# Kernel optimization log

Measured on AMD Instinct MI355X. Metric: run time of the kernel, lower is better.

Reference implementation:

```python
import jax, jax.numpy as jnp
import numpy as np

B, T, N, C = 64, 256, 21, 3
HID, HEADS, HDIM, DOUT = 128, 4, 32, 256
CDIM, DMODEL = 64, 256
DINNER, DSTATE, DCONV, DTRANK, L = 512, 16, 4, 16, 4
NSIGNS, NHS, NLOC, NMOV, NORI = 2000, 40, 20, 20, 8
TEMP = 0.07

def _ln(x, w):
    mu = x.mean(-1, keepdims=True)
    var = ((x - mu) ** 2).mean(-1, keepdims=True)
    return (x - mu) / jnp.sqrt(var + 1e-5) * w

def _silu(x):
    return x * jax.nn.sigmoid(x)

def _causal_conv(u, w, b):  # u:(B,T,D), depthwise causal conv, w:(D,K)
    K = w.shape[1]
    up = jnp.pad(u, ((0, 0), (K - 1, 0), (0, 0)))
    y = sum(up[:, k:k + u.shape[1], :] * w[:, k] for k in range(K))
    return y + b

def _scan(u, dt, Bm, Cm, A, Dp):  # selective SSM scan; u,dt:(B,T,Di), Bm,Cm:(B,T,Ds)
    def step(h, xs):
        dt_t, b_t, c_t, u_t = xs
        dA = jnp.exp(dt_t[..., None] * A)                       # (B,Di,Ds)
        dBu = dt_t[..., None] * b_t[:, None, :] * u_t[..., None]
        h = dA * h + dBu
        y = jnp.einsum('bds,bs->bd', h, c_t)
        return h, y
    h0 = jnp.zeros((u.shape[0], A.shape[0], A.shape[1]), u.dtype)
    xs = (dt.swapaxes(0, 1), Bm.swapaxes(0, 1), Cm.swapaxes(0, 1), u.swapaxes(0, 1))
    _, ys = jax.lax.scan(step, h0, xs)
    return ys.swapaxes(0, 1) + u * Dp

def _cos_logits(f, p):
    fn = f / (jnp.linalg.norm(f, axis=-1, keepdims=True) + 1e-8)
    pn = p / (jnp.linalg.norm(p, axis=-1, keepdims=True) + 1e-8)
    return fn @ pn.T / TEMP

def _forward(x, agan_w_in, agan_b_in, agan_w_gat, agan_a_src, agan_a_dst,
             agan_w_out, agan_b_out, pdm_w, pdm_b, pdm_w_fuse, pdm_b_fuse,
             ssm_ln_w, ssm_in_proj, ssm_conv_w, ssm_conv_b, ssm_x_proj,
             ssm_dt_w, ssm_dt_b, ssm_A_log, ssm_D, ssm_out_proj,
             hpc_w_sign, hpc_b_sign, sign_protos, proto_hs, proto_loc,
             proto_mov, proto_ori):
    # ---- AGAN: multi-head graph attention over N landmarks per frame ----
    h0 = jax.nn.relu(x @ agan_w_in + agan_b_in)                  # (B,T,N,HID)
    h = jnp.einsum('btni,hio->btnho', h0, agan_w_gat)            # (B,T,N,H,O)
    src = jnp.einsum('btnho,ho->btnh', h, agan_a_src)
    dst = jnp.einsum('btnho,ho->btnh', h, agan_a_dst)
    e = jax.nn.leaky_relu(src[:, :, :, None, :] + dst[:, :, None, :, :], 0.2)  # (B,T,Ni,Nj,H)
    alpha = jax.nn.softmax(e, axis=3)
    agg = jnp.einsum('btijh,btjho->btiho', alpha, h).reshape(h0.shape)
    feat = jax.nn.relu(h0 + agg)
    spatial = (feat @ agan_w_out + agan_b_out).mean(axis=2)      # (B,T,DOUT)
    # ---- PDM: 4 phonological component projections + fusion ----
    comps = jax.nn.relu(jnp.einsum('btd,kdc->btkc', spatial, pdm_w) + pdm_b)  # (B,T,4,CDIM)
    fused = comps.reshape(B, T, 4 * CDIM) @ pdm_w_fuse + pdm_b_fuse           # (B,T,DMODEL)
    # ---- BiSSM: bidirectional selective SSM layers with residuals ----
    xx = fused
    for l in range(L):
        xn = _ln(xx, ssm_ln_w[l])
        ysum = 0.0
        for d in range(2):
            u_in = xn if d == 0 else xn[:, ::-1]
            xz = u_in @ ssm_in_proj[l, d]
            u, z = xz[..., :DINNER], xz[..., DINNER:]
            u = _silu(_causal_conv(u, ssm_conv_w[l, d], ssm_conv_b[l, d]))
            xdbl = u @ ssm_x_proj[l, d]
            dt = jax.nn.softplus(xdbl[..., :DTRANK] @ ssm_dt_w[l, d] + ssm_dt_b[l, d])
            Bm = xdbl[..., DTRANK:DTRANK + DSTATE]
            Cm = xdbl[..., DTRANK + DSTATE:]
            A = -jnp.exp(ssm_A_log[l, d])
            y = _scan(u, dt, Bm, Cm, A, ssm_D[l, d]) * _silu(z)
            y = y @ ssm_out_proj[l, d]
            ysum = ysum + (y if d == 0 else y[:, ::-1])
        xx = xx + ysum
    temporal = xx
    # ---- HPC: prototype classifier ----
    emb = temporal.mean(axis=1) @ hpc_w_sign + hpc_b_sign        # (B,DMODEL)
    logits = _cos_logits(emb, sign_protos)                       # (B,NSIGNS)
    pooled_c = comps.mean(axis=1)                                # (B,4,CDIM)
    sims = tuple(_cos_logits(pooled_c[:, k], p)
                 for k, p in enumerate((proto_hs, proto_loc, proto_mov, proto_ori)))
    return (logits, emb) + sims

def setup_inputs():
    key = jax.random.key(0)
    ks = iter(jax.random.split(key, 40))
    def rn(shape, scale):
        return jax.random.normal(next(ks), shape, jnp.float32) * scale
    inp = {}
    inp['x'] = rn((B, T, N, C), 1.0)
    inp['agan_w_in'] = rn((C, HID), C ** -0.5)
    inp['agan_b_in'] = jnp.zeros((HID,), jnp.float32)
    inp['agan_w_gat'] = rn((HEADS, HID, HDIM), HID ** -0.5)
    inp['agan_a_src'] = rn((HEADS, HDIM), 0.1)
    inp['agan_a_dst'] = rn((HEADS, HDIM), 0.1)
    inp['agan_w_out'] = rn((HID, DOUT), HID ** -0.5)
    inp['agan_b_out'] = jnp.zeros((DOUT,), jnp.float32)
    inp['pdm_w'] = rn((4, DOUT, CDIM), DOUT ** -0.5)
    inp['pdm_b'] = jnp.zeros((4, CDIM), jnp.float32)
    inp['pdm_w_fuse'] = rn((4 * CDIM, DMODEL), (4 * CDIM) ** -0.5)
    inp['pdm_b_fuse'] = jnp.zeros((DMODEL,), jnp.float32)
    inp['ssm_ln_w'] = jnp.ones((L, DMODEL), jnp.float32)
    inp['ssm_in_proj'] = rn((L, 2, DMODEL, 2 * DINNER), DMODEL ** -0.5)
    inp['ssm_conv_w'] = rn((L, 2, DINNER, DCONV), DCONV ** -0.5)
    inp['ssm_conv_b'] = jnp.zeros((L, 2, DINNER), jnp.float32)
    inp['ssm_x_proj'] = rn((L, 2, DINNER, DTRANK + 2 * DSTATE), DINNER ** -0.5)
    inp['ssm_dt_w'] = rn((L, 2, DTRANK, DINNER), DTRANK ** -0.5)
    inp['ssm_dt_b'] = jnp.full((L, 2, DINNER), -4.6, jnp.float32)  # softplus ~ 0.01
    a = jnp.log(jnp.tile(jnp.arange(1, DSTATE + 1, dtype=jnp.float32)[None, :], (DINNER, 1)))
    inp['ssm_A_log'] = jnp.tile(a[None, None], (L, 2, 1, 1))
    inp['ssm_D'] = jnp.ones((L, 2, DINNER), jnp.float32)
    inp['ssm_out_proj'] = rn((L, 2, DINNER, DMODEL), DINNER ** -0.5)
    inp['hpc_w_sign'] = rn((DMODEL, DMODEL), DMODEL ** -0.5)
    inp['hpc_b_sign'] = jnp.zeros((DMODEL,), jnp.float32)
    inp['sign_protos'] = rn((NSIGNS, DMODEL), 1.0)
    inp['proto_hs'] = rn((NHS, CDIM), 1.0)
    inp['proto_loc'] = rn((NLOC, CDIM), 1.0)
    inp['proto_mov'] = rn((NMOV, CDIM), 1.0)
    inp['proto_ori'] = rn((NORI, CDIM), 1.0)
    return inp

def reference(x, agan_w_in, agan_b_in, agan_w_gat, agan_a_src, agan_a_dst,
              agan_w_out, agan_b_out, pdm_w, pdm_b, pdm_w_fuse, pdm_b_fuse,
              ssm_ln_w, ssm_in_proj, ssm_conv_w, ssm_conv_b, ssm_x_proj,
              ssm_dt_w, ssm_dt_b, ssm_A_log, ssm_D, ssm_out_proj,
              hpc_w_sign, hpc_b_sign, sign_protos, proto_hs, proto_loc,
              proto_mov, proto_ori):
    return _forward(x, agan_w_in, agan_b_in, agan_w_gat, agan_a_src, agan_a_dst,
                    agan_w_out, agan_b_out, pdm_w, pdm_b, pdm_w_fuse, pdm_b_fuse,
                    ssm_ln_w, ssm_in_proj, ssm_conv_w, ssm_conv_b, ssm_x_proj,
                    ssm_dt_w, ssm_dt_b, ssm_A_log, ssm_D, ssm_out_proj,
                    hpc_w_sign, hpc_b_sign, sign_protos, proto_hs, proto_loc,
                    proto_mov, proto_ori)
```

## Files before the change

### kernel.cpp

```cpp
#include <hip/hip_runtime.h>
#include <hip/hip_bf16.h>
#include <math.h>

#define BB 64
#define TT 256
#define NNODE 21
#define HID 128
#define DMODEL 256
#define DINNER 512
#define NSIGNS 2000
#define BTT (BB*TT)

typedef unsigned short u16;
typedef unsigned int u32;
typedef __attribute__((ext_vector_type(8))) short short8;
typedef __attribute__((ext_vector_type(4))) float f32x4;

template<int V> struct IC { static constexpr int v = V; };

__device__ __forceinline__ float siluf(float x){ return x/(1.f+expf(-x)); }
__device__ __forceinline__ u16 f2bf(float x){ __hip_bfloat16 h = __float2bfloat16(x); return *(u16*)&h; }
__device__ __forceinline__ u32 pk2bf(float a, float b){
  float2 f2; f2.x = a; f2.y = b;
  __hip_bfloat162 h2 = __float22bfloat162_rn(f2);
  return *(u32*)&h2;
}
__device__ __forceinline__ float bf2f(u16 u){ return __uint_as_float(((u32)u)<<16); }
__device__ __forceinline__ void gload16(const u16* g, u16* l){
  __builtin_amdgcn_global_load_lds((const __attribute__((address_space(1))) void*)g,
                                   (__attribute__((address_space(3))) void*)l, 16, 0, 0);
}

__global__ __launch_bounds__(256) void transpose_w_kernel(
    const float* __restrict__ in_proj, const float* __restrict__ out_proj,
    const float* __restrict__ x_proj, const float* __restrict__ w_out,
    const float* __restrict__ pdm_w, const float* __restrict__ w_fuse,
    const float* __restrict__ w_gat, u16* __restrict__ dst)
{
  __shared__ short tl[64*66];
  int bx = blockIdx.x, tid = threadIdx.x;
  const float* S = nullptr; size_t soff = 0; int lds = 0, Nsrc = 0;
  size_t doff = 0; int ldd = 0, Nout = 0;
  int tn = 0, tk = 0;
  bool zero = false;
  if (bx < 512) {
    int j = bx >> 5, tt = bx & 31;
    int l = j >> 2, d = j & 1, zh = (j >> 1) & 1;
    tn = tt >> 2; tk = tt & 3;
    S = in_proj; soff = ((size_t)(l*2+d)*256)*1024 + zh*512; lds = 1024; Nsrc = 512;
    doff = (size_t)l*524288 + (size_t)(zh*1024 + d*512)*256; ldd = 256; Nout = 512;
  } else if (bx < 768) {
    int j = (bx-512) >> 5, tt = (bx-512) & 31;
    int l = j >> 1, d = j & 1;
    tn = tt >> 3; tk = tt & 7;
    S = out_proj; soff = (size_t)(l*2+d)*512*256; lds = 256; Nsrc = 256;
    doff = 2097152 + (size_t)l*262144 + d*512; ldd = 1024; Nout = 256;
  } else if (bx < 896) {
    int j = (bx-768) >> 3, tt = (bx-768) & 7;
    int l = j >> 2, sub = j & 3;
    tn = 0; tk = tt;
    if (sub < 2) {
      int d = sub;
      S = x_proj; soff = (size_t)(l*2+d)*512*48; lds = 48; Nsrc = 48;
      doff = 3145728 + (size_t)l*131072 + (size_t)(d*64)*1024 + d*512; ldd = 1024; Nout = 64;
    } else {
      int d = sub-2; zero = true;
      doff = 3145728 + (size_t)l*131072 + (size_t)(d*64)*1024 + (1-d)*512; ldd = 1024; Nout = 64;
    }
  } else if (bx < 904) {
    int tt = bx-896; tn = tt>>1; tk = tt&1;
    S = w_out; soff = 0; lds = 256; Nsrc = 256;
    doff = 3670016; ldd = 128; Nout = 256;
  } else if (bx < 920) {
    int j = (bx-904)>>2, tt = (bx-904)&3;
    tn = 0; tk = tt;
    S = pdm_w; soff = (size_t)j*16384; lds = 64; Nsrc = 64;
    doff = 3702784 + (size_t)j*16384; ldd = 256; Nout = 64;
  } else if (bx < 936) {
    int tt = bx-920; tn = tt>>2; tk = tt&3;
    S = w_fuse; soff = 0; lds = 256; Nsrc = 256;
    doff = 3768320; ldd = 256; Nout = 256;
  } else {
    int j = (bx-936)>>1, tt = (bx-936)&1;
    tn = 0; tk = tt;
    S = w_gat; soff = (size_t)j*4096; lds = 32; Nsrc = 32;
    doff = 3833856 + (size_t)j*4096; ldd = 128; Nout = 32;
  }
  int n0 = tn*64, k0 = tk*64;
  if (!zero) {
    #pragma unroll
    for (int i=0;i<16;++i){
      int kk = i*4 + (tid>>6), nn = tid&63;
      float v = (n0+nn < Nsrc) ? S[soff + (size_t)(k0+kk)*lds + n0+nn] : 0.f;
      tl[nn*66+kk] = (short)f2bf(v);
    }
    __syncthreads();
    #pragma unroll
    for (int i=0;i<16;++i){
      int nn = i*4 + (tid>>6), kk = tid&63;
      if (n0+nn < Nout) dst[doff + (size_t)(n0+nn)*ldd + k0+kk] = (u16)tl[nn*66+kk];
    }
  } else {
    #pragma unroll
    for (int i=0;i<16;++i){
      int nn = i*4 + (tid>>6), kk = tid&63;
      if (n0+nn < Nout) dst[doff + (size_t)(n0+nn)*ldd + k0+kk] = 0;
    }
  }
}

__global__ __launch_bounds__(256) void agan_kernel(
    const float* __restrict__ x, const float* __restrict__ w_in, const float* __restrict__ b_in,
    const u16* __restrict__ bpt, const float* __restrict__ a_src, const float* __restrict__ a_dst,
    u16* __restrict__ fsum_out)
{
  int bt = blockIdx.x;
  int tid = threadIdx.x;
  int lane = tid & 63, wid = tid >> 6;
  int lr = lane & 15, lq = lane >> 4;
  __shared__ float xv[NNODE][4];
  __shared__ __align__(16) short sh0[32*136];
  __shared__ __align__(16) short hmT[128*40];
  __shared__ __align__(16) short alb[4*32*40];
  __shared__ float sd[2][NNODE][4];
  __shared__ float sm[4][NNODE];
  short8 bp[4][2];
  #pragma unroll
  for (int ks=0;ks<4;++ks)
    #pragma unroll
    for (int ct=0;ct<2;++ct)
      bp[ks][ct] = *(const short8*)(bpt + (size_t)(wid*32+ct*16+lr)*128 + ks*32 + lq*8);
  float as0 = a_src[wid*32 + lr],      as1 = a_src[wid*32 + 16 + lr];
  float ad0 = a_dst[wid*32 + lr],      ad1 = a_dst[wid*32 + 16 + lr];
  if (tid < NNODE*3) xv[tid/3][tid%3] = x[(size_t)bt*63 + tid];
  __syncthreads();
  for (int idx = tid; idx < 32*128; idx += 256) {
    int n = idx >> 7, i = idx & 127;
    float v = 0.f;
    if (n < NNODE)
      v = fmaxf(b_in[i] + xv[n][0]*w_in[i] + xv[n][1]*w_in[128+i] + xv[n][2]*w_in[256+i], 0.f);
    sh0[n*136 + i] = (short)f2bf(v);
  }
  __syncthreads();
  {
    f32x4 g00={},g01={},g10={},g11={};
    #pragma unroll
    for (int ks=0;ks<4;++ks){
      short8 a0 = *(const short8*)&sh0[(lr   )*136 + ks*32 + lq*8];
      short8 a1 = *(const short8*)&sh0[(16+lr)*136 + ks*32 + lq*8];
      g00 = __builtin_amdgcn_mfma_f32_16x16x32_bf16(a0, bp[ks][0], g00, 0,0,0);
      g01 = __builtin_amdgcn_mfma_f32_16x16x32_bf16(a0, bp[ks][1], g01, 0,0,0);
      g10 = __builtin_amdgcn_mfma_f32_16x16x32_bf16(a1, bp[ks][0], g10, 0,0,0);
      g11 = __builtin_amdgcn_mfma_f32_16x16x32_bf16(a1, bp[ks][1], g11, 0,0,0);
    }
    f32x4 gg[2][2] = {{g00,g01},{g10,g11}};
    #pragma unroll
    for (int mt=0;mt<2;++mt)
      #pragma unroll
      for (int ct=0;ct<2;++ct){
        int col = wid*32 + ct*16 + lr;
        int row0 = mt*16 + lq*4;
        u32 w0 = pk2bf(gg[mt][ct][0], gg[mt][ct][1]);
        u32 w1 = pk2bf(gg[mt][ct][2], gg[mt][ct][3]);
        *(uint2*)&hmT[col*40 + row0] = make_uint2(w0,w1);
      }
    #pragma unroll
    for (int mt=0;mt<2;++mt)
      #pragma unroll
      for (int r=0;r<4;++r){
        float ps = gg[mt][0][r]*as0 + gg[mt][1][r]*as1;
        float pd = gg[mt][0][r]*ad0 + gg[mt][1][r]*ad1;
        #pragma unroll
        for (int off=1; off<16; off<<=1){
          ps += __shfl_xor(ps, off);
          pd += __shfl_xor(pd, off);
        }
        int n = mt*16 + lq*4 + r;
        if (lr == 0 && n < NNODE){ sd[0][n][wid] = ps; sd[1][n][wid] = pd; }
      }
  }
  __syncthreads();
  if (tid < 84) {
    int i = tid >> 2, h = tid & 3;
    float sv = sd[0][i][h], m = -1e30f;
    #pragma unroll
    for (int j=0;j<NNODE;++j){
      float e = sv + sd[1][j][h];
      e = e>=0.f ? e : 0.2f*e;
      m = fmaxf(m,e);
    }
    sm[h][i] = m;
  }
  __syncthreads();
  for (int idx = tid; idx < 84*32; idx += 256) {
    int j = idx & 31, ih = idx >> 5;
    int i = ih >> 2, h = ih & 3;
    float ex = 0.f;
    if (j < NNODE){
      float e = sd[0][i][h] + sd[1][j][h];
      e = e>=0.f ? e : 0.2f*e;
      ex = __expf(e - sm[h][i]);
    }
    alb[(h*32+i)*40 + j] = (short)f2bf(ex);
  }
  __syncthreads();
  if (tid < 84) {
    int i = tid >> 2, h = tid & 3;
    const short* row = &alb[(h*32+i)*40];
    float s = 0.f;
    #pragma unroll
    for (int j=0;j<NNODE;++j) s += bf2f((u16)row[j]);
    sm[h][i] = 1.f/s;
  }
  __syncthreads();
  {
    int h = wid;
    short8 a0 = *(const short8*)&alb[(h*32 + lr     )*40 + lq*8];
    short8 a1 = *(const short8*)&alb[(h*32 + 16 + lr)*40 + lq*8];
    short8 b0 = *(const short8*)&hmT[(h*32 + lr     )*40 + lq*8];
    short8 b1 = *(const short8*)&hmT[(h*32 + 16 + lr)*40 + lq*8];
    f32x4 c00={},c01={},c10={},c11={};
    c00 = __builtin_amdgcn_mfma_f32_16x16x32_bf16(a0,b0,c00,0,0,0);
    c01 = __builtin_amdgcn_mfma_f32_16x16x32_bf16(a0,b1,c01,0,0,0);
    c10 = __builtin_amdgcn_mfma_f32_16x16x32_bf16(a1,b0,c10,0,0,0);
    c11 = __builtin_amdgcn_mfma_f32_16x16x32_bf16(a1,b1,c11,0,0,0);
    f32x4 cc[2][2] = {{c00,c01},{c10,c11}};
    #pragma unroll
    for (int ct=0; ct<2; ++ct){
      int col = h*32 + ct*16 + lr;
      float s = 0.f;
      #pragma unroll
      for (int mt=0; mt<2; ++mt)
        #pragma unroll
        for (int r=0;r<4;++r){
          int n = mt*16 + lq*4 + r;
          if (n < NNODE)
            s += fmaxf(bf2f((u16)sh0[n*136+col]) + cc[mt][ct][r]*sm[h][n], 0.f);
        }
      s += __shfl_xor(s, 16);
      s += __shfl_xor(s, 32);
      if (lq == 0) fsum_out[(size_t)bt*128 + col] = f2bf(s*(1.f/21.f));
    }
  }
}

template<int ACC, int BIAS, int RELU, int SM>
__global__ __launch_bounds__(256) void gemm_bf16_kernel(
    const u16* __restrict__ A, const u16* __restrict__ BT, const float* __restrict__ bias,
    float* __restrict__ C, u16* __restrict__ C2,
    int M, int N, int K, int lda)
{
  __shared__ __align__(16) short Asl[8192];
  __shared__ __align__(16) short Bsl[8192];
  int tid = threadIdx.x;
  int lane = tid & 63, wid = tid >> 6;
  int wm = wid >> 1, wn = wid & 1;
  int row0 = blockIdx.y*128, col0 = blockIdx.x*128;
  const u16* Ab = A  + (size_t)row0*lda;
  const u16* Bb = BT + (size_t)col0*K;
  f32x4 acc[4][4] = {};
  int lrow = lane & 15, lk = (lane>>4)*8;
  for (int k0 = 0; k0 < K; k0 += 64) {
    #pragma unroll
    for (int is=0; is<4; ++is){
      int li = is*256 + tid;
      int row = li >> 3;
      int c8  = (li & 7) ^ (row & 7);
      gload16(Ab + (size_t)row*lda + k0 + c8*8, (u16*)Asl + ((is<<8)+(wid<<6))*8);
      gload16(Bb + (size_t)row*K   + k0 + c8*8, (u16*)Bsl + ((is<<8)+(wid<<6))*8);
    }
    __syncthreads();
    #pragma unroll
    for (int ksub=0; ksub<2; ++ksub){
      int slot = (ksub*32 + lk) >> 3;
      short8 a[4], b[4];
      #pragma unroll
      for (int i=0;i<4;++i){ int rr=wm*64+i*16+lrow; a[i]=*(const short8*)&Asl[rr*64+((slot^(rr&7))<<3)]; }
      #pragma unroll
      for (int j=0;j<4;++j){ int rr=wn*64+j*16+lrow; b[j]=*(const short8*)&Bsl[rr*64+((slot^(rr&7))<<3)]; }
      #pragma unroll
      for (int i=0;i<4;++i)
        #pragma unroll
        for (int j=0;j<4;++j)
          acc[i][j] = __builtin_amdgcn_mfma_f32_16x16x32_bf16(a[i], b[j], acc[i][j], 0, 0, 0);
    }
    __syncthreads();
  }
  #pragma unroll
  for (int i=0;i<4;++i) {
    int row = row0 + wm*64 + i*16 + (lane>>4)*4;
    #pragma unroll
    for (int j=0;j<4;++j) {
      int col = col0 + wn*64 + j*16 + (lane&15);
      if (col < N) {
        float bv = BIAS ? bias[col] : 0.f;
        #pragma unroll
        for (int r=0;r<4;++r) {
          float v = acc[i][j][r] + bv;
          if (RELU) v = fmaxf(v, 0.f);
          size_t o = (size_t)(row+r)*N + col;
          if (ACC)           C[o] += v;
          else if (SM == 0)  C[o]  = v;
          else               C2[o] = f2bf(v);
        }
      }
    }
  }
}

template<int ACC, int BIAS, int RELU, int SM, int POOL>
__global__ __launch_bounds__(256) void gemm_bm64_kernel(
    const u16* __restrict__ A, const u16* __restrict__ BT, const float* __restrict__ bias,
    float* __restrict__ C, u16* __restrict__ C2, float* __restrict__ pool,
    int M, int N, int K, int lda)
{
  __shared__ __align__(16) short Asl[4096];
  __shared__ __align__(16) short Bsl[8192];
  int tid = threadIdx.x;
  int lane = tid & 63, wid = tid >> 6;
  int wm = wid >> 1, wn = wid & 1;
  int row0 = blockIdx.y*64, col0 = blockIdx.x*128;
  const u16* Ab = A  + (size_t)row0*lda;
  const u16* Bb = BT + (size_t)col0*K;
  f32x4 acc[2][4] = {};
  int lrow = lane & 15, lq = lane >> 4, lk = lq*8;
  for (int k0 = 0; k0 < K; k0 += 64) {
    #pragma unroll
    for (int is=0; is<2; ++is){
      int li = is*256 + tid;
      int row = li >> 3;
      int c8  = (li & 7) ^ (row & 7);
      gload16(Ab + (size_t)row*lda + k0 + c8*8, (u16*)Asl + ((is<<8)+(wid<<6))*8);
    }
    #pragma unroll
    for (int is=0; is<4; ++is){
      int li = is*256 + tid;
      int row = li >> 3;
      int c8  = (li & 7) ^ (row & 7);
      gload16(Bb + (size_t)row*K + k0 + c8*8, (u16*)Bsl + ((is<<8)+(wid<<6))*8);
    }
    __syncthreads();
    #pragma unroll
    for (int ksub=0; ksub<2; ++ksub){
      int slot = (ksub*32 + lk) >> 3;
      short8 a[2], b[4];
      #pragma unroll
      for (int i=0;i<2;++i){ int rr=wm*32+i*16+lrow; a[i]=*(const short8*)&Asl[rr*64+((slot^(rr&7))<<3)]; }
      #pragma unroll
      for (int j=0;j<4;++j){ int rr=wn*64+j*16+lrow; b[j]=*(const short8*)&Bsl[rr*64+((slot^(rr&7))<<3)]; }
      #pragma unroll
      for (int i=0;i<2;++i)
        #pragma unroll
        for (int j=0;j<4;++j)
          acc[i][j] = __builtin_amdgcn_mfma_f32_16x16x32_bf16(a[i], b[j], acc[i][j], 0, 0, 0);
    }
    __syncthreads();
  }
  float colsum[4] = {0.f,0.f,0.f,0.f};
  #pragma unroll
  for (int i=0;i<2;++i) {
    int row = row0 + wm*32 + i*16 + lq*4;
    #pragma unroll
    for (int j=0;j<4;++j) {
      int col = col0 + wn*64 + j*16 + lrow;
      if (col < N) {
        float bv = BIAS ? bias[col] : 0.f;
        #pragma unroll
        for (int r=0;r<4;++r) {
          float v = acc[i][j][r] + bv;
          if (RELU) v = fmaxf(v, 0.f);
          size_t o = (size_t)(row+r)*N + col;
          if (ACC)           C[o] += v;
          else if (SM == 0)  C[o]  = v;
          else               C2[o] = f2bf(v);
          if (POOL) colsum[j] += v;
        }
      }
    }
  }
  if (POOL) {
    float* red = (float*)Asl;
    #pragma unroll
    for (int j=0;j<4;++j) red[tid*4+j] = colsum[j];
    __syncthreads();
    if (tid < 128) {
      int wn_ = tid >> 6, j_ = (tid >> 4) & 3, l15 = tid & 15;
      float s = 0.f;
      #pragma unroll
      for (int wm_=0;wm_<2;++wm_)
        #pragma unroll
        for (int g=0;g<4;++g)
          s += red[(((wm_*2+wn_)*64) + g*16 + l15)*4 + j_];
      pool[(size_t)blockIdx.y*256 + blockIdx.x*128 + tid] = s * (1.f/256.f);
    }
  }
}

__global__ __launch_bounds__(256) void ln_kernel(const float* __restrict__ x,
    const float* __restrict__ w, u16* __restrict__ o)
{
  int row = blockIdx.x*4 + (threadIdx.x>>6);
  int lane = threadIdx.x & 63;
  float4 v = *(const float4*)(x + (size_t)row*DMODEL + lane*4);
  float s = v.x+v.y+v.z+v.w;
  #pragma unroll
  for (int off=32;off>=1;off>>=1) s += __shfl_xor(s, off);
  float mu = s * (1.f/256.f);
  float d0=v.x-mu, d1=v.y-mu, d2=v.z-mu, d3=v.w-mu;
  float q = d0*d0+d1*d1+d2*d2+d3*d3;
  #pragma unroll
  for (int off=32;off>=1;off>>=1) q += __shfl_xor(q, off);
  float inv = 1.f/sqrtf(q*(1.f/256.f) + 1e-5f);
  float4 wv = *(const float4*)(w + lane*4);
  uint2 pk; pk.x = pk2bf(d0*inv*wv.x, d1*inv*wv.y); pk.y = pk2bf(d2*inv*wv.z, d3*inv*wv.w);
  *(uint2*)(o + (size_t)row*DMODEL + lane*4) = pk;
}

__global__ __launch_bounds__(256) void conv_kernel(const u16* __restrict__ xz,
    const float* __restrict__ cw, const float* __restrict__ cb,
    u16* __restrict__ ucv)
{
  int idx = blockIdx.x*256 + threadIdx.x;
  int du8 = idx & 127, dir = du8 >> 6, d8 = (du8 & 63) << 3;
  int bt = idx >> 7, t = bt & 255;
  const u16* up = xz + (size_t)(bt - t)*2048 + dir*512 + d8;
  float w[8][4];
  #pragma unroll
  for (int j=0;j<8;++j){
    float4 wv = *(const float4*)(cw + (size_t)dir*2048 + (d8+j)*4);
    w[j][0]=wv.x; w[j][1]=wv.y; w[j][2]=wv.z; w[j][3]=wv.w;
  }
  float s[8];
  float4 cb0 = *(const float4*)(cb + dir*512 + d8);
  float4 cb1 = *(const float4*)(cb + dir*512 + d8 + 4);
  s[0]=cb0.x; s[1]=cb0.y; s[2]=cb0.z; s[3]=cb0.w;
  s[4]=cb1.x; s[5]=cb1.y; s[6]=cb1.z; s[7]=cb1.w;
  if (dir == 0) {
    #pragma unroll
    for (int k=0;k<4;++k){
      int tk = t-3+k;
      if (tk >= 0){
        short8 uv = *(const short8*)(up + (size_t)tk*2048);
        #pragma unroll
        for (int j=0;j<8;++j) s[j] += w[j][k]*bf2f((u16)uv[j]);
      }
    }
  } else {
    #pragma unroll
    for (int kk=0;kk<4;++kk){
      int tk = t+kk;
      if (tk < TT){
        short8 uv = *(const short8*)(up + (size_t)tk*2048);
        #pragma unroll
        for (int j=0;j<8;++j) s[j] += w[j][3-kk]*bf2f((u16)uv[j]);
      }
    }
  }
  short8 o;
  #pragma unroll
  for (int j=0;j<8;++j) o[j] = (short)f2bf(siluf(s[j]));
  *(short8*)(ucv + (size_t)bt*1024 + dir*512 + d8) = o;
}

template<int FINAL>
__global__ __launch_bounds__(256) void scan_phase_kernel(
    const u16* __restrict__ ucv, const float* __restrict__ xd, const u16* __restrict__ xz,
    const float* __restrict__ dtw, const float* __restrict__ dtb,
    const float* __restrict__ alog, const float* __restrict__ dvec,
    const u16* __restrict__ hend_r, const float* __restrict__ sdt_r,
    float* __restrict__ sdt_w, u16* __restrict__ hend_w,
    u16* __restrict__ yout)
{
  int b = blockIdx.x, c = blockIdx.y, gz = blockIdx.z;
  int d = gz >> 1;
  int tid = threadIdx.x;
  int dd = ((gz & 1) << 8) + tid;
  float wdt[16], Av[16], h[16];
  #pragma unroll
  for (int s=0;s<16;++s){
    wdt[s] = dtw[d*8192 + s*512 + dd];
    Av[s]  = -__expf(alog[d*8192 + dd*16 + s]);
    h[s]   = 0.f;
  }
  float bdt = dtb[d*512 + dd];
  bool powok = true;
  #pragma unroll
  for (int s=0;s<16;++s) powok = powok && (fabsf(Av[s] + (float)(s+1)) < 1e-5f*(float)(s+1));
  __shared__ float sxd[32][48];
  for (int i = tid; i < 1536; i += 256){
    int q = i/48, r = i - q*48;
    int p = (c<<5)+q, t = d ? 255-p : p;
    sxd[q][r] = xd[((size_t)b*TT + t)*128 + d*64 + r];
  }
  if (FINAL) {
    for (int cp=0; cp<c; ++cp){
      size_t cbase = (((size_t)b*8+cp)*2+d)*512 + dd;
      float S = sdt_r[cbase];
      short8 h0v = *(const short8*)(hend_r + cbase*16);
      short8 h1v = *(const short8*)(hend_r + cbase*16 + 8);
      #pragma unroll
      for (int s=0;s<8;++s)  h[s]   = fmaf(__expf(Av[s]*S),   h[s],   bf2f((u16)h0v[s]));
      #pragma unroll
      for (int s=0;s<8;++s)  h[s+8] = fmaf(__expf(Av[s+8]*S), h[s+8], bf2f((u16)h1v[s]));
    }
  }
  __syncthreads();
  float S = 0.f;
  float Dv = FINAL ? dvec[d*512 + dd] : 0.f;
  const u16* ub = ucv + d*512 + dd;
  const u16* zb = xz + 1024 + d*512 + dd;
  u16* yb = yout + d*512 + dd;
  auto qloop = [&](auto icpow){
    constexpr int POW = decltype(icpow)::v;
    #pragma unroll 4
    for (int q=0;q<32;++q) {
      int p = (c<<5)+q, t = d ? 255-p : p;
      size_t row = (size_t)b*TT + t;
      float uc = bf2f(ub[row*1024]);
      float zc = FINAL ? bf2f(zb[row*2048]) : 0.f;
      const float* sr = sxd[q];
      float p0=0.f,p1=0.f,p2=0.f,p3=0.f;
      #pragma unroll
      for (int r=0;r<16;r+=4){
        p0 = fmaf(sr[r+0],wdt[r+0],p0);
        p1 = fmaf(sr[r+1],wdt[r+1],p1);
        p2 = fmaf(sr[r+2],wdt[r+2],p2);
        p3 = fmaf(sr[r+3],wdt[r+3],p3);
      }
      float dtp = bdt + ((p0+p1)+(p2+p3));
      float dt = fmaxf(dtp,0.f) + __logf(1.f + __expf(-fabsf(dtp)));
      float dtu = dt*uc;
      if (!FINAL) S += dt;
      float y0=0.f, y1=0.f;
      if (POW) {
        float rr = __expf(-dt);
        float pw = rr;
        #pragma unroll
        for (int s=0;s<16;++s){
          h[s] = fmaf(pw, h[s], dtu*sr[16+s]);
          if (FINAL) y0 = fmaf(h[s], sr[32+s], y0);
          pw *= rr;
        }
      } else {
        #pragma unroll
        for (int s=0;s<16;s+=2){
          float dA0 = __expf(dt*Av[s]);
          float dA1 = __expf(dt*Av[s+1]);
          h[s]   = fmaf(dA0, h[s],   dtu*sr[16+s]);
          h[s+1] = fmaf(dA1, h[s+1], dtu*sr[16+s+1]);
          if (FINAL){ y0 = fmaf(h[s],sr[32+s],y0); y1 = fmaf(h[s+1],sr[32+s+1],y1); }
        }
      }
      if (FINAL){
        float yv = (y0+y1) + uc*Dv;
        float sg = zc / (1.f + __expf(-zc));
        yb[row*2048] = f2bf(yv*sg);
      }
    }
  };
  if (powok) qloop(IC<1>{}); else qloop(IC<0>{});
  if (!FINAL){
    size_t co = (((size_t)b*8+c)*2+d)*512 + dd;
    sdt_w[co] = S;
    short8 o0, o1;
    #pragma unroll
    for (int s=0;s<8;++s){ o0[s] = (short)f2bf(h[s]); o1[s] = (short)f2bf(h[s+8]); }
    *(short8*)(hend_w + co*16)     = o0;
    *(short8*)(hend_w + co*16 + 8) = o1;
  }
}

__global__ __launch_bounds__(256) void emb_kernel(const float* __restrict__ xx,
    const float* __restrict__ wsgn, const float* __restrict__ bsgn,
    float* __restrict__ embw, float* __restrict__ out)
{
  int b = blockIdx.x, tid = threadIdx.x;
  __shared__ float mt[256];
  float s0=0.f,s1=0.f,s2=0.f,s3=0.f;
  for (int t=0;t<TT;t+=4){
    s0 += xx[((size_t)b*TT+t  )*DMODEL + tid];
    s1 += xx[((size_t)b*TT+t+1)*DMODEL + tid];
    s2 += xx[((size_t)b*TT+t+2)*DMODEL + tid];
    s3 += xx[((size_t)b*TT+t+3)*DMODEL + tid];
  }
  mt[tid] = (s0+s1+s2+s3)*(1.f/256.f);
  __syncthreads();
  float acc = bsgn[tid];
  for (int i=0;i<DMODEL;++i) acc += mt[i]*wsgn[i*DMODEL + tid];
  embw[b*DMODEL+tid] = acc;
  out[128000 + b*DMODEL + tid] = acc;
}

__global__ __launch_bounds__(256) void head_kernel(const float* __restrict__ embw,
    const float* __restrict__ protos, float* __restrict__ out)
{
  int b = blockIdx.x, qt = blockIdx.y, tid = threadIdx.x;
  __shared__ __align__(16) float e[256];
  __shared__ float red[4];
  float acc = embw[b*DMODEL + tid];
  e[tid] = acc;
  __syncthreads();
  float v = acc*acc;
  #pragma unroll
  for (int off=32;off>=1;off>>=1) v += __shfl_xor(v, off);
  if ((tid&63)==0) red[tid>>6] = v;
  __syncthreads();
  float esc = 1.f/(sqrtf(red[0]+red[1]+red[2]+red[3]) + 1e-8f);
  int pend = qt*500 + 500;
  for (int p = qt*500 + tid; p < pend; p += 256) {
    const float* pr = protos + (size_t)p*256;
    float dot=0.f, ps=0.f;
    for (int i=0;i<256;i+=4) {
      float4 pv = *(const float4*)(pr+i);
      float4 ev = *(const float4*)(e+i);
      dot += pv.x*ev.x + pv.y*ev.y + pv.z*ev.z + pv.w*ev.w;
      ps  += pv.x*pv.x + pv.y*pv.y + pv.z*pv.z + pv.w*pv.w;
    }
    out[(size_t)b*NSIGNS + p] = dot*esc/(sqrtf(ps)+1e-8f)*(1.f/0.07f);
  }
}

__global__ __launch_bounds__(256) void sims_kernel(const float* __restrict__ part,
    const float* __restrict__ phs, const float* __restrict__ ploc,
    const float* __restrict__ pmov, const float* __restrict__ pori,
    float* __restrict__ out)
{
  int b = blockIdx.x, tid = threadIdx.x;
  __shared__ float pc[256];
  __shared__ float nk[4];
  pc[tid] = part[(size_t)(4*b)*256 + tid] + part[(size_t)(4*b+1)*256 + tid]
          + part[(size_t)(4*b+2)*256 + tid] + part[(size_t)(4*b+3)*256 + tid];
  __syncthreads();
  if (tid < 4) {
    float ss = 0.f;
    for (int i=0;i<64;++i){ float q = pc[tid*64+i]; ss += q*q; }
    nk[tid] = 1.f/(sqrtf(ss)+1e-8f);
  }
  __syncthreads();
  if (tid < 88) {
    int k, pi; const float* P; size_t off; int npk;
    if (tid < 40)      { k=0; pi=tid;    P=phs;  off=144384; npk=40; }
    else if (tid < 60) { k=1; pi=tid-40; P=ploc; off=146944; npk=20; }
    else if (tid < 80) { k=2; pi=tid-60; P=pmov; off=148224; npk=20; }
    else               { k=3; pi=tid-80; P=pori; off=149504; npk=8;  }
    float dot=0.f, ps=0.f;
    for (int i=0;i<64;++i){ float pv = P[pi*64+i]; dot += pv*pc[k*64+i]; ps += pv*pv; }
    out[off + (size_t)b*npk + pi] = dot*nk[k]/(sqrtf(ps)+1e-8f)*(1.f/0.07f);
  }
}

extern "C" void kernel_launch(void* const* d_in, const int* in_sizes, int n_in,
                              void* d_out, int out_size, void* d_ws, size_t ws_size,
                              hipStream_t stream) {
  const float* x         = (const float*)d_in[0];
  const float* w_in      = (const float*)d_in[1];
  const float* b_in      = (const float*)d_in[2];
  const float* w_gat     = (const float*)d_in[3];
  const float* a_src     = (const float*)d_in[4];
  const float* a_dst     = (const float*)d_in[5];
  const float* w_out     = (const float*)d_in[6];
  const float* b_out     = (const float*)d_in[7];
  const float* pdm_w     = (const float*)d_in[8];
  const float* pdm_b     = (const float*)d_in[9];
  const float* w_fuse    = (const float*)d_in[10];
  const float* b_fuse    = (const float*)d_in[11];
  const float* ln_w      = (const float*)d_in[12];
  const float* in_proj   = (const float*)d_in[13];
  const float* conv_w    = (const float*)d_in[14];
  const float* conv_b    = (const float*)d_in[15];
  const float* x_proj    = (const float*)d_in[16];
  const float* dt_w      = (const float*)d_in[17];
  const float* dt_b      = (const float*)d_in[18];
  const float* A_log     = (const float*)d_in[19];
  const float* Dvec      = (const float*)d_in[20];
  const float* out_proj  = (const float*)d_in[21];
  const float* w_sign    = (const float*)d_in[22];
  const float* b_sign    = (const float*)d_in[23];
  const float* protos    = (const float*)d_in[24];
  const float* phs       = (const float*)d_in[25];
  const float* ploc      = (const float*)d_in[26];
  const float* pmov      = (const float*)d_in[27];
  const float* pori      = (const float*)d_in[28];
  float* out = (float*)d_out;

  float* wsf = (float*)d_ws;
  const size_t f_xx    = 0;
  const size_t f_xdbl  = f_xx   + 4194304;
  const size_t f_part  = f_xdbl + 2097152;
  const size_t f_emb   = f_part + 65536;
  const size_t f_end   = f_emb  + 16384;
  u16* wsu = (u16*)(wsf + f_end);
  const size_t u_xn    = 0;
  const size_t u_xz    = u_xn   + 4194304;
  const size_t u_ucv   = u_xz   + 33554432;
  const size_t u_fsum  = u_ucv  + 16777216;
  const size_t u_spat  = u_fsum + 2097152;
  const size_t u_comps = u_spat + 4194304;
  const size_t u_w     = u_comps+ 4194304;
  u16* wiT = wsu + u_w;
  u16* woT = wiT + 2097152;
  u16* wxT = woT + 1048576;
  u16* wA  = wxT + 524288;
  u16* wB  = wA  + 32768;
  u16* wF  = wB  + 65536;
  u16* wBp = wF  + 65536;
  u16*   hstate = wsu + u_fsum;
  float* sdt    = (float*)(wsu + u_fsum + 8388608);

  transpose_w_kernel<<<944, 256, 0, stream>>>(in_proj, out_proj, x_proj, w_out, pdm_w, w_fuse, w_gat, wsu + u_w);
  agan_kernel<<<BTT, 256, 0, stream>>>(x, w_in, b_in, wBp, a_src, a_dst, wsu + u_fsum);
  gemm_bm64_kernel<0,1,0,1,0><<<dim3(2,256), 256, 0, stream>>>(wsu+u_fsum, wA, b_out, nullptr, wsu+u_spat, nullptr, BTT, 256, 128, 128);
  gemm_bm64_kernel<0,1,1,1,1><<<dim3(2,256), 256, 0, stream>>>(wsu+u_spat, wB, pdm_b, nullptr, wsu+u_comps, wsf+f_part, BTT, 256, 256, 256);
  gemm_bm64_kernel<0,1,0,0,0><<<dim3(2,256), 256, 0, stream>>>(wsu+u_comps, wF, b_fuse, wsf+f_xx, nullptr, nullptr, BTT, 256, 256, 256);

  for (int l = 0; l < 4; ++l) {
    ln_kernel<<<BTT/4, 256, 0, stream>>>(wsf+f_xx, ln_w + l*DMODEL, wsu+u_xn);
    gemm_bf16_kernel<0,0,0,1><<<dim3(16,128), 256, 0, stream>>>(wsu+u_xn, wiT + (size_t)l*524288,
        nullptr, nullptr, wsu+u_xz, BTT, 2048, 256, 256);
    conv_kernel<<<BTT*128/256, 256, 0, stream>>>(wsu+u_xz, conv_w + (size_t)l*4096,
        conv_b + (size_t)l*1024, wsu+u_ucv);
    gemm_bm64_kernel<0,0,0,0,0><<<dim3(1,256), 256, 0, stream>>>(wsu+u_ucv, wxT + (size_t)l*131072,
        nullptr, wsf+f_xdbl, nullptr, nullptr, BTT, 128, 1024, 1024);
    scan_phase_kernel<0><<<dim3(64,7,4), 256, 0, stream>>>(wsu+u_ucv, wsf+f_xdbl, nullptr,
        dt_w + (size_t)l*16384, dt_b + (size_t)l*1024,
        A_log + (size_t)l*16384, nullptr,
        nullptr, nullptr, sdt, hstate, nullptr);
    scan_phase_kernel<1><<<dim3(64,8,4), 256, 0, stream>>>(wsu+u_ucv, wsf+f_xdbl, wsu+u_xz,
        dt_w + (size_t)l*16384, dt_b + (size_t)l*1024,
        A_log + (size_t)l*16384, Dvec + (size_t)l*1024,
        hstate, sdt, nullptr, nullptr, wsu+u_xz);
    gemm_bm64_kernel<1,0,0,0,0><<<dim3(2,256), 256, 0, stream>>>(wsu+u_xz, woT + (size_t)l*262144,
        nullptr, wsf+f_xx, nullptr, nullptr, BTT, 256, 1024, 2048);
  }

  emb_kernel<<<64, 256, 0, stream>>>(wsf+f_xx, w_sign, b_sign, wsf+f_emb, out);
  head_kernel<<<dim3(64,4), 256, 0, stream>>>(wsf+f_emb, protos, out);
  sims_kernel<<<64, 256, 0, stream>>>(wsf+f_part, phs, ploc, pmov, pori, out);
  (void)in_sizes; (void)n_in; (void)out_size; (void)ws_size;
}
```

Baseline: 1.181 ms.

## Streamline AGAN attention, add 64-wide x_proj GEMM, merge sims into head kernel

In the AGAN kernel, the input-projection weights are hoisted into registers. The src/dst attention scores are now computed from the bf16 hmT tile in shared memory instead of shuffle reductions, and the softmax row sum is folded into the exp loop with a wave shuffle, which removes one barrier stage. A new 64x64-tile GEMM kernel replaces the N=128 single-column-block GEMM for x_proj, giving the grid twice as many blocks. The sims kernel is merged into head_kernel as an extra grid row to save a launch. Computing the scores from bf16-rounded values slightly changes numerics.

```diff
diff --git a/kernel.cpp b/kernel.cpp
--- a/kernel.cpp
+++ b/kernel.cpp
@@ -130,16 +130,17 @@
     #pragma unroll
     for (int ct=0;ct<2;++ct)
       bp[ks][ct] = *(const short8*)(bpt + (size_t)(wid*32+ct*16+lr)*128 + ks*32 + lq*8);
-  float as0 = a_src[wid*32 + lr],      as1 = a_src[wid*32 + 16 + lr];
-  float ad0 = a_dst[wid*32 + lr],      ad1 = a_dst[wid*32 + 16 + lr];
+  int ii = tid & 127, nn0 = tid >> 7;
+  float w0 = w_in[ii], w1 = w_in[128+ii], w2 = w_in[256+ii], bi = b_in[ii];
   if (tid < NNODE*3) xv[tid/3][tid%3] = x[(size_t)bt*63 + tid];
   __syncthreads();
-  for (int idx = tid; idx < 32*128; idx += 256) {
-    int n = idx >> 7, i = idx & 127;
+  #pragma unroll
+  for (int n = 0; n < 32; n += 2) {
+    int nr = n + nn0;
     float v = 0.f;
-    if (n < NNODE)
-      v = fmaxf(b_in[i] + xv[n][0]*w_in[i] + xv[n][1]*w_in[128+i] + xv[n][2]*w_in[256+i], 0.f);
-    sh0[n*136 + i] = (short)f2bf(v);
+    if (nr < NNODE)
+      v = fmaxf(bi + xv[nr][0]*w0 + xv[nr][1]*w1 + xv[nr][2]*w2, 0.f);
+    sh0[nr*136 + ii] = (short)f2bf(v);
   }
   __syncthreads();
   {
@@ -160,24 +161,21 @@
       for (int ct=0;ct<2;++ct){
         int col = wid*32 + ct*16 + lr;
         int row0 = mt*16 + lq*4;
-        u32 w0 = pk2bf(gg[mt][ct][0], gg[mt][ct][1]);
-        u32 w1 = pk2bf(gg[mt][ct][2], gg[mt][ct][3]);
-        *(uint2*)&hmT[col*40 + row0] = make_uint2(w0,w1);
-      }
-    #pragma unroll
-    for (int mt=0;mt<2;++mt)
-      #pragma unroll
-      for (int r=0;r<4;++r){
-        float ps = gg[mt][0][r]*as0 + gg[mt][1][r]*as1;
-        float pd = gg[mt][0][r]*ad0 + gg[mt][1][r]*ad1;
-        #pragma unroll
-        for (int off=1; off<16; off<<=1){
-          ps += __shfl_xor(ps, off);
-          pd += __shfl_xor(pd, off);
-        }
-        int n = mt*16 + lq*4 + r;
-        if (lr == 0 && n < NNODE){ sd[0][n][wid] = ps; sd[1][n][wid] = pd; }
-      }
+        u32 wv0 = pk2bf(gg[mt][ct][0], gg[mt][ct][1]);
+        u32 wv1 = pk2bf(gg[mt][ct][2], gg[mt][ct][3]);
+        *(uint2*)&hmT[col*40 + row0] = make_uint2(wv0,wv1);
+      }
+  }
+  __syncthreads();
+  if (tid < 168) {
+    int which = tid >= 84;
+    int r = tid - which*84;
+    int n = r >> 2, h = r & 3;
+    const float* av = (which ? a_dst : a_src) + h*32;
+    float s = 0.f;
+    #pragma unroll
+    for (int o=0;o<32;++o){ int oo=(o+tid)&31; s += bf2f((u16)hmT[(h*32+oo)*40 + n])*av[oo]; }
+    sd[which][n][h] = s;
   }
   __syncthreads();
   if (tid < 84) {
@@ -195,22 +193,18 @@
   for (int idx = tid; idx < 84*32; idx += 256) {
     int j = idx & 31, ih = idx >> 5;
     int i = ih >> 2, h = ih & 3;
+    float m = sm[h][i];
     float ex = 0.f;
     if (j < NNODE){
       float e = sd[0][i][h] + sd[1][j][h];
       e = e>=0.f ? e : 0.2f*e;
-      ex = __expf(e - sm[h][i]);
+      ex = __expf(e - m);
     }
     alb[(h*32+i)*40 + j] = (short)f2bf(ex);
-  }
-  __syncthreads();
-  if (tid < 84) {
-    int i = tid >> 2, h = tid & 3;
-    const short* row = &alb[(h*32+i)*40];
-    float s = 0.f;
-    #pragma unroll
-    for (int j=0;j<NNODE;++j) s += bf2f((u16)row[j]);
-    sm[h][i] = 1.f/s;
+    float s = ex;
+    #pragma unroll
+    for (int off=1; off<32; off<<=1) s += __shfl_xor(s, off);
+    if (j == 0) sm[h][i] = 1.f/s;
   }
   __syncthreads();
   {
@@ -392,6 +386,54 @@
         for (int g=0;g<4;++g)
           s += red[(((wm_*2+wn_)*64) + g*16 + l15)*4 + j_];
       pool[(size_t)blockIdx.y*256 + blockIdx.x*128 + tid] = s * (1.f/256.f);
+    }
+  }
+}
+
+__global__ __launch_bounds__(256) void gemm_n64_kernel(
+    const u16* __restrict__ A, const u16* __restrict__ BT,
+    float* __restrict__ C, int N, int K, int lda)
+{
+  __shared__ __align__(16) short Asl[4096];
+  __shared__ __align__(16) short Bsl[4096];
+  int tid = threadIdx.x;
+  int lane = tid & 63, wid = tid >> 6;
+  int lrow = lane & 15, lq = lane >> 4, lk = lq*8;
+  int row0 = blockIdx.y*64, col0 = blockIdx.x*64;
+  const u16* Ab = A  + (size_t)row0*lda;
+  const u16* Bb = BT + (size_t)col0*K;
+  f32x4 acc[4] = {};
+  for (int k0 = 0; k0 < K; k0 += 64) {
+    #pragma unroll
+    for (int is=0; is<2; ++is){
+      int li = is*256 + tid;
+      int row = li >> 3;
+      int c8  = (li & 7) ^ (row & 7);
+      gload16(Ab + (size_t)row*lda + k0 + c8*8, (u16*)Asl + ((is<<8)+(wid<<6))*8);
+      gload16(Bb + (size_t)row*K   + k0 + c8*8, (u16*)Bsl + ((is<<8)+(wid<<6))*8);
+    }
+    __syncthreads();
+    #pragma unroll
+    for (int ksub=0; ksub<2; ++ksub){
+      int slot = (ksub*32 + lk) >> 3;
+      int arr = wid*16 + lrow;
+      short8 av = *(const short8*)&Asl[arr*64 + ((slot^(arr&7))<<3)];
+      #pragma unroll
+      for (int j=0;j<4;++j){
+        int brr = j*16 + lrow;
+        short8 bv = *(const short8*)&Bsl[brr*64 + ((slot^(brr&7))<<3)];
+        acc[j] = __builtin_amdgcn_mfma_f32_16x16x32_bf16(av, bv, acc[j], 0, 0, 0);
+      }
+    }
+    __syncthreads();
+  }
+  #pragma unroll
+  for (int j=0;j<4;++j){
+    int col = col0 + j*16 + lrow;
+    #pragma unroll
+    for (int r=0;r<4;++r){
+      int row = row0 + wid*16 + lq*4 + r;
+      C[(size_t)row*N + col] = acc[j][r];
     }
   }
 }
@@ -592,11 +634,36 @@
 }
 
 __global__ __launch_bounds__(256) void head_kernel(const float* __restrict__ embw,
-    const float* __restrict__ protos, float* __restrict__ out)
+    const float* __restrict__ protos, const float* __restrict__ part,
+    const float* __restrict__ phs, const float* __restrict__ ploc,
+    const float* __restrict__ pmov, const float* __restrict__ pori,
+    float* __restrict__ out)
 {
   int b = blockIdx.x, qt = blockIdx.y, tid = threadIdx.x;
   __shared__ __align__(16) float e[256];
   __shared__ float red[4];
+  if (qt == 4) {
+    e[tid] = part[(size_t)(4*b)*256 + tid] + part[(size_t)(4*b+1)*256 + tid]
+           + part[(size_t)(4*b+2)*256 + tid] + part[(size_t)(4*b+3)*256 + tid];
+    __syncthreads();
+    if (tid < 4) {
+      float ss = 0.f;
+      for (int i=0;i<64;++i){ float q = e[tid*64+i]; ss += q*q; }
+      red[tid] = 1.f/(sqrtf(ss)+1e-8f);
+    }
+    __syncthreads();
+    if (tid < 88) {
+      int k, pi; const float* P; size_t off; int npk;
+      if (tid < 40)      { k=0; pi=tid;    P=phs;  off=144384; npk=40; }
+      else if (tid < 60) { k=1; pi=tid-40; P=ploc; off=146944; npk=20; }
+      else if (tid < 80) { k=2; pi=tid-60; P=pmov; off=148224; npk=20; }
+      else               { k=3; pi=tid-80; P=pori; off=149504; npk=8;  }
+      float dot=0.f, ps=0.f;
+      for (int i=0;i<64;++i){ float pv = P[pi*64+i]; dot += pv*e[k*64+i]; ps += pv*pv; }
+      out[off + (size_t)b*npk + pi] = dot*red[k]/(sqrtf(ps)+1e-8f)*(1.f/0.07f);
+    }
+    return;
+  }
   float acc = embw[b*DMODEL + tid];
   e[tid] = acc;
   __syncthreads();
@@ -617,35 +684,6 @@
       ps  += pv.x*pv.x + pv.y*pv.y + pv.z*pv.z + pv.w*pv.w;
     }
     out[(size_t)b*NSIGNS + p] = dot*esc/(sqrtf(ps)+1e-8f)*(1.f/0.07f);
-  }
-}
-
-__global__ __launch_bounds__(256) void sims_kernel(const float* __restrict__ part,
-    const float* __restrict__ phs, const float* __restrict__ ploc,
-    const float* __restrict__ pmov, const float* __restrict__ pori,
-    float* __restrict__ out)
-{
-  int b = blockIdx.x, tid = threadIdx.x;
-  __shared__ float pc[256];
-  __shared__ float nk[4];
-  pc[tid] = part[(size_t)(4*b)*256 + tid] + part[(size_t)(4*b+1)*256 + tid]
-          + part[(size_t)(4*b+2)*256 + tid] + part[(size_t)(4*b+3)*256 + tid];
-  __syncthreads();
-  if (tid < 4) {
-    float ss = 0.f;
-    for (int i=0;i<64;++i){ float q = pc[tid*64+i]; ss += q*q; }
-    nk[tid] = 1.f/(sqrtf(ss)+1e-8f);
-  }
-  __syncthreads();
-  if (tid < 88) {
-    int k, pi; const float* P; size_t off; int npk;
-    if (tid < 40)      { k=0; pi=tid;    P=phs;  off=144384; npk=40; }
-    else if (tid < 60) { k=1; pi=tid-40; P=ploc; off=146944; npk=20; }
-    else if (tid < 80) { k=2; pi=tid-60; P=pmov; off=148224; npk=20; }
-    else               { k=3; pi=tid-80; P=pori; off=149504; npk=8;  }
-    float dot=0.f, ps=0.f;
-    for (int i=0;i<64;++i){ float pv = P[pi*64+i]; dot += pv*pc[k*64+i]; ps += pv*pv; }
-    out[off + (size_t)b*npk + pi] = dot*nk[k]/(sqrtf(ps)+1e-8f)*(1.f/0.07f);
   }
 }
 
@@ -719,8 +757,8 @@
         nullptr, nullptr, wsu+u_xz, BTT, 2048, 256, 256);
     conv_kernel<<<BTT*128/256, 256, 0, stream>>>(wsu+u_xz, conv_w + (size_t)l*4096,
         conv_b + (size_t)l*1024, wsu+u_ucv);
-    gemm_bm64_kernel<0,0,0,0,0><<<dim3(1,256), 256, 0, stream>>>(wsu+u_ucv, wxT + (size_t)l*131072,
-        nullptr, wsf+f_xdbl, nullptr, nullptr, BTT, 128, 1024, 1024);
+    gemm_n64_kernel<<<dim3(2,256), 256, 0, stream>>>(wsu+u_ucv, wxT + (size_t)l*131072,
+        wsf+f_xdbl, 128, 1024, 1024);
     scan_phase_kernel<0><<<dim3(64,7,4), 256, 0, stream>>>(wsu+u_ucv, wsf+f_xdbl, nullptr,
         dt_w + (size_t)l*16384, dt_b + (size_t)l*1024,
         A_log + (size_t)l*16384, nullptr,
@@ -734,7 +772,6 @@
   }
 
   emb_kernel<<<64, 256, 0, stream>>>(wsf+f_xx, w_sign, b_sign, wsf+f_emb, out);
-  head_kernel<<<dim3(64,4), 256, 0, stream>>>(wsf+f_emb, protos, out);
-  sims_kernel<<<64, 256, 0, stream>>>(wsf+f_part, phs, ploc, pmov, pori, out);
+  head_kernel<<<dim3(64,5), 256, 0, stream>>>(wsf+f_emb, protos, wsf+f_part, phs, ploc, pmov, pori, out);
   (void)in_sizes; (void)n_in; (void)out_size; (void)ws_size;
 }
```

Result: faster. 1.151 ms (-2.5%).
